# Kernel optimization log

Hardware: AMD Instinct MI355X
Metric: run time of the kernel (lower is better)

The kernel has to match this reference:

```python
import jax, jax.numpy as jnp
import numpy as np

B, S, D = 4, 2048, 1024
H = 16
HD = D // H  # head_dim = key_dim = value_dim = 64


def setup_inputs() -> dict:
    key = jax.random.key(0)
    ks = jax.random.split(key, 4)
    scale = (2.0 / (D + D)) ** 0.5  # xavier_normal for square weight
    return {
        "hidden_states": jax.random.normal(ks[0], (B, S, D), dtype=jnp.float32),
        "Wq": jax.random.normal(ks[1], (D, D), dtype=jnp.float32) * scale,
        "bq": jnp.zeros((D,), dtype=jnp.float32),
        "Wk": jax.random.normal(ks[2], (D, D), dtype=jnp.float32) * scale,
        "bk": jnp.zeros((D,), dtype=jnp.float32),
        "Wv": jax.random.normal(ks[3], (D, D), dtype=jnp.float32) * scale,
        "bv": jnp.zeros((D,), dtype=jnp.float32),
    }


def _split_heads(x):
    # [B, S, H*HD] -> [B, H, S, HD]
    b, s, _ = x.shape
    return x.reshape(b, s, H, HD).transpose(0, 2, 1, 3)


def reference(hidden_states, Wq, bq, Wk, bk, Wv, bv):
    # Linear projections (torch Linear: x @ W.T + b)
    q = _split_heads(hidden_states @ Wq.T + bq)  # [B,H,S,HD]
    k = _split_heads(hidden_states @ Wk.T + bk)
    v = _split_heads(hidden_states @ Wv.T + bv)
    scores = jnp.einsum("bhqd,bhkd->bhqk", q, k) / jnp.sqrt(jnp.float32(HD))
    probs = jax.nn.softmax(scores, axis=-1)
    out = jnp.einsum("bhqk,bhkd->bhqd", probs, v)  # [B,H,S,HD]
    # merge heads -> [B, S, H*HD]
    return out.transpose(0, 2, 1, 3).reshape(B, S, H * HD)
```

## Files before the change

### kernel.cpp

```cpp
#include <hip/hip_runtime.h>
#include <math.h>

#define SB 4
#define SS 2048
#define SD 1024
#define SH 16
#define SHD 64
#define SM (SB * SS)

using f32x4 = __attribute__((ext_vector_type(4))) float;
using h8    = __attribute__((ext_vector_type(8))) _Float16;
using h4    = __attribute__((ext_vector_type(4))) _Float16;
using fp16x2 = __fp16 __attribute__((ext_vector_type(2)));
using fp16x4 = __fp16 __attribute__((ext_vector_type(4)));

__device__ __forceinline__ unsigned short f2h(float x) {
  _Float16 h = (_Float16)x;
  return __builtin_bit_cast(unsigned short, h);
}

__device__ __forceinline__ void gld_lds16(const unsigned short* g, unsigned short* l) {
  __builtin_amdgcn_global_load_lds(
      (const __attribute__((address_space(1))) unsigned int*)g,
      (__attribute__((address_space(3))) unsigned int*)l, 16, 0, 0);
}

__global__ __launch_bounds__(256) void cvt4h(const float* __restrict__ in,
                                             unsigned short* __restrict__ out, int n4) {
  int i = blockIdx.x * 256 + threadIdx.x;
  if (i >= n4) return;
  float4 v = ((const float4*)in)[i];
  unsigned long long r = (unsigned long long)f2h(v.x)
                       | ((unsigned long long)f2h(v.y) << 16)
                       | ((unsigned long long)f2h(v.z) << 32)
                       | ((unsigned long long)f2h(v.w) << 48);
  ((unsigned long long*)out)[i] = r;
}

__global__ __launch_bounds__(256) void cvt3w(const float* __restrict__ w0, const float* __restrict__ w1,
                                             const float* __restrict__ w2,
                                             unsigned short* __restrict__ o0, unsigned short* __restrict__ o1,
                                             unsigned short* __restrict__ o2) {
  const int z = blockIdx.y;
  const float* in = (z == 0) ? w0 : (z == 1) ? w1 : w2;
  unsigned short* out = (z == 0) ? o0 : (z == 1) ? o1 : o2;
  int i = blockIdx.x * 256 + threadIdx.x;
  float4 v = ((const float4*)in)[i];
  unsigned long long r = (unsigned long long)f2h(v.x)
                       | ((unsigned long long)f2h(v.y) << 16)
                       | ((unsigned long long)f2h(v.z) << 32)
                       | ((unsigned long long)f2h(v.w) << 48);
  ((unsigned long long*)out)[i] = r;
}

__global__ __launch_bounds__(256) void gemm_qkv(
    const unsigned short* __restrict__ Xh,
    const unsigned short* __restrict__ Wqh, const unsigned short* __restrict__ Wkh,
    const unsigned short* __restrict__ Wvh,
    const float* __restrict__ bq, const float* __restrict__ bk, const float* __restrict__ bv,
    unsigned short* __restrict__ Qh, unsigned short* __restrict__ Kh,
    unsigned short* __restrict__ Vt) {
  __shared__ unsigned short lA[128 * 64];
  __shared__ unsigned short lB[128 * 64];
  const int z = blockIdx.z;
  const unsigned short* W = (z == 0) ? Wqh : (z == 1) ? Wkh : Wvh;
  const float* bias = (z == 0) ? bq : (z == 1) ? bk : bv;

  const int tid = threadIdx.x;
  const int wave = tid >> 6, lane = tid & 63;
  const int quad = lane >> 4, l16 = lane & 15;
  const int tN = blockIdx.x * 128, tM = blockIdx.y * 128;
  const int wr = (wave >> 1) * 64, wc = (wave & 1) * 64;

  f32x4 acc[4][4] = {};

  const int rB = tid >> 3;
  const int colOff = (((tid & 7) ^ (rB & 7))) * 8;
  const unsigned short* gA[4];
  const unsigned short* gB[4];
#pragma unroll
  for (int i = 0; i < 4; ++i) {
    gA[i] = Xh + (size_t)(tM + i * 32 + rB) * SD + colOff;
    gB[i] = W  + (size_t)(tN + i * 32 + rB) * SD + colOff;
  }
  unsigned short* dA[4];
  unsigned short* dB[4];
#pragma unroll
  for (int i = 0; i < 4; ++i) {
    dA[i] = lA + (i * 256 + wave * 64) * 8;
    dB[i] = lB + (i * 256 + wave * 64) * 8;
  }
  const int swl = l16 & 7;

  for (int k0 = 0; k0 < SD; k0 += 64) {
    __syncthreads();
#pragma unroll
    for (int i = 0; i < 4; ++i) gld_lds16(gA[i] + k0, dA[i]);
#pragma unroll
    for (int i = 0; i < 4; ++i) gld_lds16(gB[i] + k0, dB[i]);
    __syncthreads();

#pragma unroll
    for (int ks = 0; ks < 2; ++ks) {
      h8 af[4], bf[4];
#pragma unroll
      for (int mi = 0; mi < 4; ++mi)
        af[mi] = *(const h8*)(lA + (wr + mi * 16 + l16) * 64 + (((ks * 4 + quad) ^ swl) * 8));
#pragma unroll
      for (int ni = 0; ni < 4; ++ni)
        bf[ni] = *(const h8*)(lB + (wc + ni * 16 + l16) * 64 + (((ks * 4 + quad) ^ swl) * 8));
#pragma unroll
      for (int mi = 0; mi < 4; ++mi)
#pragma unroll
        for (int ni = 0; ni < 4; ++ni)
          acc[mi][ni] = __builtin_amdgcn_mfma_f32_16x16x32_f16(af[mi], bf[ni], acc[mi][ni], 0, 0, 0);
    }
  }

  if (z == 2) {
#pragma unroll
    for (int ni = 0; ni < 4; ++ni) {
      const int gn = tN + wc + ni * 16 + l16;
      const float bb = bias[gn];
#pragma unroll
      for (int mi = 0; mi < 4; ++mi) {
        const int gm = tM + wr + mi * 16 + quad * 4;
        const int vb = gm >> 11, vs = gm & 2047;
        unsigned long long wv = 0;
#pragma unroll
        for (int r = 0; r < 4; ++r)
          wv |= (unsigned long long)f2h(acc[mi][ni][r] + bb) << (16 * r);
        *(unsigned long long*)(Vt + (size_t)(vb * 1024 + gn) * SS + vs) = wv;
      }
    }
  } else {
    const float sc = (z == 0) ? 0.18033688011112042f : 1.0f;
    unsigned short* C = (z == 0) ? Qh : Kh;
#pragma unroll
    for (int ni = 0; ni < 4; ++ni) {
      const int gn = tN + wc + ni * 16 + l16;
      const float bb = bias[gn];
#pragma unroll
      for (int mi = 0; mi < 4; ++mi)
#pragma unroll
        for (int r = 0; r < 4; ++r) {
          const int gm = tM + wr + mi * 16 + quad * 4 + r;
          C[(size_t)gm * SD + gn] = f2h((acc[mi][ni][r] + bb) * sc);
        }
    }
  }
}

__global__ __launch_bounds__(256, 4) void attn(const unsigned short* __restrict__ Qh,
                                               const unsigned short* __restrict__ Kh,
                                               const unsigned short* __restrict__ Vt,
                                               float* __restrict__ out) {
  __shared__ unsigned short lK[2][64 * 64];
  __shared__ unsigned short lV[2][64 * 64];
  const int tid = threadIdx.x;
  const int wave = tid >> 6, lane = tid & 63;
  const int quad = lane >> 4, l16 = lane & 15;
  const int bid = blockIdx.x;
  const int bh = (bid & 7) | (((bid >> 3) & 7) << 3);
  const int qt = bid >> 6;
  const int b = bh >> 4, h = bh & 15;
  const int qs = qt * 64 + wave * 16;

  const unsigned short* qp = Qh + ((size_t)(b * SS + qs + l16)) * SD + h * 64 + quad * 8;
  h8 aq0 = *(const h8*)(qp);
  h8 aq1 = *(const h8*)(qp + 32);

  const int row0 = tid >> 3, cs0 = (tid & 7) ^ (row0 & 7);
  const int row1 = row0 + 32, cs1 = (tid & 7) ^ (row1 & 7);
  const unsigned short* kS0 = Kh + ((size_t)(b * SS + row0)) * SD + h * 64 + cs0 * 8;
  const unsigned short* kS1 = Kh + ((size_t)(b * SS + row1)) * SD + h * 64 + cs1 * 8;
  const unsigned short* vS0 = Vt + ((size_t)(bh * 64 + row0)) * SS + cs0 * 8;
  const unsigned short* vS1 = Vt + ((size_t)(bh * 64 + row1)) * SS + cs1 * 8;
  unsigned short* dK0 = &lK[0][wave * 512];
  unsigned short* dK1 = &lK[0][2048 + wave * 512];
  unsigned short* dV0 = &lV[0][wave * 512];
  unsigned short* dV1 = &lV[0][2048 + wave * 512];

  f32x4 ov[4] = {};
  float l_acc = 0.f;
  const int swl = l16 & 7;

  gld_lds16(kS0, dK0); gld_lds16(kS1, dK1);
  gld_lds16(vS0, dV0); gld_lds16(vS1, dV1);
  kS0 += 64 * SD; kS1 += 64 * SD; vS0 += 64; vS1 += 64;

  for (int kt = 0; kt < 32; ++kt) {
    const int buf = kt & 1;
    __syncthreads();
    if (kt < 31) {
      const int o = (buf ^ 1) * 64 * 64;
      gld_lds16(kS0, dK0 + o); gld_lds16(kS1, dK1 + o);
      gld_lds16(vS0, dV0 + o); gld_lds16(vS1, dV1 + o);
      kS0 += 64 * SD; kS1 += 64 * SD; vS0 += 64; vS1 += 64;
    }
    const unsigned short* Kt = lK[buf];
    const unsigned short* Vl = lV[buf];

    f32x4 s[4];
#pragma unroll
    for (int nt = 0; nt < 4; ++nt) {
      const unsigned short* kr = Kt + (nt * 16 + l16) * 64;
      h8 kf0 = *(const h8*)(kr + ((quad ^ swl) * 8));
      h8 kf1 = *(const h8*)(kr + (((4 + quad) ^ swl) * 8));
      f32x4 z = {};
      z = __builtin_amdgcn_mfma_f32_16x16x32_f16(kf0, aq0, z, 0, 0, 0);
      s[nt] = __builtin_amdgcn_mfma_f32_16x16x32_f16(kf1, aq1, z, 0, 0, 0);
    }
    h4 vf[4][4];
#pragma unroll
    for (int nt = 0; nt < 4; ++nt)
#pragma unroll
      for (int f = 0; f < 4; ++f)
        vf[nt][f] = *(const h4*)(Vl + (f * 16 + l16) * 64 +
                                 (((nt * 2 + (quad >> 1)) ^ swl) * 8) + (quad & 1) * 4);
#pragma unroll
    for (int nt = 0; nt < 4; ++nt) {
      float p0 = __builtin_amdgcn_exp2f(s[nt][0]);
      float p1 = __builtin_amdgcn_exp2f(s[nt][1]);
      float p2 = __builtin_amdgcn_exp2f(s[nt][2]);
      float p3 = __builtin_amdgcn_exp2f(s[nt][3]);
      l_acc += (p0 + p1) + (p2 + p3);
      fp16x2 lo = __builtin_amdgcn_cvt_pkrtz(p0, p1);
      fp16x2 hi = __builtin_amdgcn_cvt_pkrtz(p2, p3);
      fp16x4 pp4 = __builtin_shufflevector(lo, hi, 0, 1, 2, 3);
      h4 pp = __builtin_bit_cast(h4, pp4);
#pragma unroll
      for (int f = 0; f < 4; ++f)
        ov[f] = __builtin_amdgcn_mfma_f32_16x16x16f16(vf[nt][f], pp, ov[f], 0, 0, 0);
    }
  }
  float lt = l_acc;
  lt += __shfl_xor(lt, 16);
  lt += __shfl_xor(lt, 32);
  const float inv = 1.0f / lt;
  float* orow = out + ((size_t)(b * SS + qs + l16)) * SD + h * 64 + quad * 4;
#pragma unroll
  for (int f = 0; f < 4; ++f) {
    float4 w;
    w.x = ov[f][0] * inv; w.y = ov[f][1] * inv;
    w.z = ov[f][2] * inv; w.w = ov[f][3] * inv;
    *(float4*)(orow + f * 16) = w;
  }
}

extern "C" void kernel_launch(void* const* d_in, const int* in_sizes, int n_in,
                              void* d_out, int out_size, void* d_ws, size_t ws_size,
                              hipStream_t stream) {
  const float* hs = (const float*)d_in[0];
  const float* Wq = (const float*)d_in[1];
  const float* bq = (const float*)d_in[2];
  const float* Wk = (const float*)d_in[3];
  const float* bk = (const float*)d_in[4];
  const float* Wv = (const float*)d_in[5];
  const float* bv = (const float*)d_in[6];
  float* out = (float*)d_out;

  char* ws = (char*)d_ws;
  unsigned short* Xh  = (unsigned short*)(ws);
  unsigned short* Wqh = (unsigned short*)(ws + 16777216);
  unsigned short* Wkh = (unsigned short*)(ws + 16777216 + 2097152);
  unsigned short* Wvh = (unsigned short*)(ws + 16777216 + 2 * 2097152);
  unsigned short* Qh  = (unsigned short*)(ws + 16777216 + 3 * 2097152);
  unsigned short* Kh  = Qh + (size_t)SM * SD;
  unsigned short* Vt  = Kh + (size_t)SM * SD;

  cvt4h<<<dim3(8192), dim3(256), 0, stream>>>(hs, Xh, SM * SD / 4);
  cvt3w<<<dim3(1024, 3), dim3(256), 0, stream>>>(Wq, Wk, Wv, Wqh, Wkh, Wvh);
  gemm_qkv<<<dim3(SD / 128, SM / 128, 3), dim3(256), 0, stream>>>(
      Xh, Wqh, Wkh, Wvh, bq, bk, bv, Qh, Kh, Vt);
  attn<<<dim3(SB * SH * (SS / 64)), dim3(256), 0, stream>>>(Qh, Kh, Vt, out);
}
```

Baseline: 273.7 us.

## Process two query tiles per attention block and remap GEMM grid for XCD locality

The attention kernel now has each wave handle two 16-row query tiles, 128 queries per block. Each K/V tile loaded into LDS is therefore reused for twice the work, halving global K/V traffic and LDS fragment reads per query. The QKV GEMM launch becomes a flat 1D grid, with the block index decoded so that consecutive blocks on the same XCD share M tiles, aiming for better L2 reuse. The costs are higher register pressure in attention, which may reduce occupancy under the launch bounds of 4, and half as many attention blocks.

```diff
diff --git a/kernel.cpp b/kernel.cpp
--- a/kernel.cpp
+++ b/kernel.cpp
@@ -62,14 +62,18 @@
     unsigned short* __restrict__ Vt) {
   __shared__ unsigned short lA[128 * 64];
   __shared__ unsigned short lB[128 * 64];
-  const int z = blockIdx.z;
+  const int L = blockIdx.x;
+  const int xcd = L & 7, rr = L >> 3;
+  const int mloc = rr & 7, widx = rr >> 3;
+  const int tNi = widx & 7, z = widx >> 3;
+  const int tM = (xcd * 8 + mloc) * 128, tN = tNi * 128;
+
   const unsigned short* W = (z == 0) ? Wqh : (z == 1) ? Wkh : Wvh;
   const float* bias = (z == 0) ? bq : (z == 1) ? bk : bv;
 
   const int tid = threadIdx.x;
   const int wave = tid >> 6, lane = tid & 63;
   const int quad = lane >> 4, l16 = lane & 15;
-  const int tN = blockIdx.x * 128, tM = blockIdx.y * 128;
   const int wr = (wave >> 1) * 64, wc = (wave & 1) * 64;
 
   f32x4 acc[4][4] = {};
@@ -160,15 +164,19 @@
   const int tid = threadIdx.x;
   const int wave = tid >> 6, lane = tid & 63;
   const int quad = lane >> 4, l16 = lane & 15;
+  const int qh = quad >> 1, ql = quad & 1;
   const int bid = blockIdx.x;
   const int bh = (bid & 7) | (((bid >> 3) & 7) << 3);
   const int qt = bid >> 6;
   const int b = bh >> 4, h = bh & 15;
-  const int qs = qt * 64 + wave * 16;
-
-  const unsigned short* qp = Qh + ((size_t)(b * SS + qs + l16)) * SD + h * 64 + quad * 8;
-  h8 aq0 = *(const h8*)(qp);
-  h8 aq1 = *(const h8*)(qp + 32);
+  const int qsA = qt * 128 + wave * 16;
+
+  const unsigned short* qpA = Qh + ((size_t)(b * SS + qsA + l16)) * SD + h * 64 + quad * 8;
+  const unsigned short* qpB = qpA + (size_t)64 * SD;
+  h8 aqA0 = *(const h8*)(qpA);
+  h8 aqA1 = *(const h8*)(qpA + 32);
+  h8 aqB0 = *(const h8*)(qpB);
+  h8 aqB1 = *(const h8*)(qpB + 32);
 
   const int row0 = tid >> 3, cs0 = (tid & 7) ^ (row0 & 7);
   const int row1 = row0 + 32, cs1 = (tid & 7) ^ (row1 & 7);
@@ -181,8 +189,8 @@
   unsigned short* dV0 = &lV[0][wave * 512];
   unsigned short* dV1 = &lV[0][2048 + wave * 512];
 
-  f32x4 ov[4] = {};
-  float l_acc = 0.f;
+  f32x4 ovA[4] = {}, ovB[4] = {};
+  float l_accA = 0.f, l_accB = 0.f;
   const int swl = l16 & 7;
 
   gld_lds16(kS0, dK0); gld_lds16(kS1, dK1);
@@ -201,50 +209,78 @@
     const unsigned short* Kt = lK[buf];
     const unsigned short* Vl = lV[buf];
 
-    f32x4 s[4];
+    f32x4 sA[4], sB[4];
 #pragma unroll
     for (int nt = 0; nt < 4; ++nt) {
       const unsigned short* kr = Kt + (nt * 16 + l16) * 64;
       h8 kf0 = *(const h8*)(kr + ((quad ^ swl) * 8));
       h8 kf1 = *(const h8*)(kr + (((4 + quad) ^ swl) * 8));
-      f32x4 z = {};
-      z = __builtin_amdgcn_mfma_f32_16x16x32_f16(kf0, aq0, z, 0, 0, 0);
-      s[nt] = __builtin_amdgcn_mfma_f32_16x16x32_f16(kf1, aq1, z, 0, 0, 0);
-    }
-    h4 vf[4][4];
-#pragma unroll
-    for (int nt = 0; nt < 4; ++nt)
-#pragma unroll
-      for (int f = 0; f < 4; ++f)
-        vf[nt][f] = *(const h4*)(Vl + (f * 16 + l16) * 64 +
-                                 (((nt * 2 + (quad >> 1)) ^ swl) * 8) + (quad & 1) * 4);
-#pragma unroll
-    for (int nt = 0; nt < 4; ++nt) {
-      float p0 = __builtin_amdgcn_exp2f(s[nt][0]);
-      float p1 = __builtin_amdgcn_exp2f(s[nt][1]);
-      float p2 = __builtin_amdgcn_exp2f(s[nt][2]);
-      float p3 = __builtin_amdgcn_exp2f(s[nt][3]);
-      l_acc += (p0 + p1) + (p2 + p3);
-      fp16x2 lo = __builtin_amdgcn_cvt_pkrtz(p0, p1);
-      fp16x2 hi = __builtin_amdgcn_cvt_pkrtz(p2, p3);
-      fp16x4 pp4 = __builtin_shufflevector(lo, hi, 0, 1, 2, 3);
-      h4 pp = __builtin_bit_cast(h4, pp4);
-#pragma unroll
-      for (int f = 0; f < 4; ++f)
-        ov[f] = __builtin_amdgcn_mfma_f32_16x16x16f16(vf[nt][f], pp, ov[f], 0, 0, 0);
-    }
-  }
-  float lt = l_acc;
-  lt += __shfl_xor(lt, 16);
-  lt += __shfl_xor(lt, 32);
-  const float inv = 1.0f / lt;
-  float* orow = out + ((size_t)(b * SS + qs + l16)) * SD + h * 64 + quad * 4;
+      f32x4 zA = {};
+      zA = __builtin_amdgcn_mfma_f32_16x16x32_f16(kf0, aqA0, zA, 0, 0, 0);
+      sA[nt] = __builtin_amdgcn_mfma_f32_16x16x32_f16(kf1, aqA1, zA, 0, 0, 0);
+      f32x4 zB = {};
+      zB = __builtin_amdgcn_mfma_f32_16x16x32_f16(kf0, aqB0, zB, 0, 0, 0);
+      sB[nt] = __builtin_amdgcn_mfma_f32_16x16x32_f16(kf1, aqB1, zB, 0, 0, 0);
+    }
+
+#pragma unroll
+    for (int g = 0; g < 4; ++g) {
+      h4 vf[4];
+#pragma unroll
+      for (int f = 0; f < 4; ++f) {
+        h8 vv = *(const h8*)(Vl + (f * 16 + l16) * 64 + (((g * 2 + qh) ^ swl) * 8));
+        h4 lo = __builtin_shufflevector(vv, vv, 0, 1, 2, 3);
+        h4 hi = __builtin_shufflevector(vv, vv, 4, 5, 6, 7);
+        vf[f] = ql ? hi : lo;
+      }
+      {
+        float p0 = __builtin_amdgcn_exp2f(sA[g][0]);
+        float p1 = __builtin_amdgcn_exp2f(sA[g][1]);
+        float p2 = __builtin_amdgcn_exp2f(sA[g][2]);
+        float p3 = __builtin_amdgcn_exp2f(sA[g][3]);
+        l_accA += (p0 + p1) + (p2 + p3);
+        fp16x2 lo = __builtin_amdgcn_cvt_pkrtz(p0, p1);
+        fp16x2 hi = __builtin_amdgcn_cvt_pkrtz(p2, p3);
+        h4 pp = __builtin_bit_cast(h4, __builtin_shufflevector(lo, hi, 0, 1, 2, 3));
+#pragma unroll
+        for (int f = 0; f < 4; ++f)
+          ovA[f] = __builtin_amdgcn_mfma_f32_16x16x16f16(vf[f], pp, ovA[f], 0, 0, 0);
+      }
+      {
+        float p0 = __builtin_amdgcn_exp2f(sB[g][0]);
+        float p1 = __builtin_amdgcn_exp2f(sB[g][1]);
+        float p2 = __builtin_amdgcn_exp2f(sB[g][2]);
+        float p3 = __builtin_amdgcn_exp2f(sB[g][3]);
+        l_accB += (p0 + p1) + (p2 + p3);
+        fp16x2 lo = __builtin_amdgcn_cvt_pkrtz(p0, p1);
+        fp16x2 hi = __builtin_amdgcn_cvt_pkrtz(p2, p3);
+        h4 pp = __builtin_bit_cast(h4, __builtin_shufflevector(lo, hi, 0, 1, 2, 3));
+#pragma unroll
+        for (int f = 0; f < 4; ++f)
+          ovB[f] = __builtin_amdgcn_mfma_f32_16x16x16f16(vf[f], pp, ovB[f], 0, 0, 0);
+      }
+    }
+  }
+  float ltA = l_accA;
+  ltA += __shfl_xor(ltA, 16);
+  ltA += __shfl_xor(ltA, 32);
+  const float invA = 1.0f / ltA;
+  float ltB = l_accB;
+  ltB += __shfl_xor(ltB, 16);
+  ltB += __shfl_xor(ltB, 32);
+  const float invB = 1.0f / ltB;
+  float* orowA = out + ((size_t)(b * SS + qsA + l16)) * SD + h * 64 + quad * 4;
+  float* orowB = orowA + (size_t)64 * SD;
 #pragma unroll
   for (int f = 0; f < 4; ++f) {
     float4 w;
-    w.x = ov[f][0] * inv; w.y = ov[f][1] * inv;
-    w.z = ov[f][2] * inv; w.w = ov[f][3] * inv;
-    *(float4*)(orow + f * 16) = w;
+    w.x = ovA[f][0] * invA; w.y = ovA[f][1] * invA;
+    w.z = ovA[f][2] * invA; w.w = ovA[f][3] * invA;
+    *(float4*)(orowA + f * 16) = w;
+    float4 u;
+    u.x = ovB[f][0] * invB; u.y = ovB[f][1] * invB;
+    u.z = ovB[f][2] * invB; u.w = ovB[f][3] * invB;
+    *(float4*)(orowB + f * 16) = u;
   }
 }
 
@@ -271,7 +307,7 @@
 
   cvt4h<<<dim3(8192), dim3(256), 0, stream>>>(hs, Xh, SM * SD / 4);
   cvt3w<<<dim3(1024, 3), dim3(256), 0, stream>>>(Wq, Wk, Wv, Wqh, Wkh, Wvh);
-  gemm_qkv<<<dim3(SD / 128, SM / 128, 3), dim3(256), 0, stream>>>(
+  gemm_qkv<<<dim3(1536), dim3(256), 0, stream>>>(
       Xh, Wqh, Wkh, Wvh, bq, bk, bv, Qh, Kh, Vt);
-  attn<<<dim3(SB * SH * (SS / 64)), dim3(256), 0, stream>>>(Qh, Kh, Vt, out);
-}
+  attn<<<dim3(SB * SH * (SS / 128)), dim3(256), 0, stream>>>(Qh, Kh, Vt, out);
+}
```

New measurement: 257.5 us. 5.9% less time.
